# Performance work log

Hardware: AMD Instinct MI355X
Metric: run time of the kernel (lower is better)

Reference implementation:

```python
import jax, jax.numpy as jnp
import numpy as np

B, T, C = 8, 2048, 1024
HEAD = 64

def setup_inputs() -> dict:
    key = jax.random.key(0)
    k1, k2 = jax.random.split(key)
    x = jax.random.normal(k1, (B, T, C), dtype=jnp.float32)
    W_qkv = jax.random.normal(k2, (C, 3 * HEAD), dtype=jnp.float32) * (C ** -0.5)
    return {"x": x, "W_qkv": W_qkv}

def reference(x, W_qkv):
    # qkv projection (bias-free Linear): [B,T,3*HEAD]
    qkv = x @ W_qkv
    q, k, v = jnp.split(qkv, 3, axis=-1)  # each [B,T,HEAD]
    # scaled dot-product scores [B,T,T]
    dots = jnp.einsum('btd,bsd->bts', q, k) * (HEAD ** -0.5)
    # causal mask (tril == keep)
    Tq = x.shape[1]
    causal = jnp.tril(jnp.ones((Tq, Tq), dtype=bool))
    dots = jnp.where(causal, dots, -jnp.inf)
    attn = jax.nn.softmax(dots, axis=-1)
    # dropout p=0.0 (eval) -> identity
    out = jnp.einsum('bts,bsd->btd', attn, v)  # [B,T,HEAD]
    return out
```

## Files before the change

kernel.cpp:

```cpp
#include <hip/hip_runtime.h>
#include <stdint.h>

#define NB 8
#define NT 2048
#define NC 1024
#define HD 64

typedef __attribute__((ext_vector_type(8)))  short s16x8;
typedef __attribute__((ext_vector_type(4)))  float f32x4;
typedef __attribute__((ext_vector_type(16))) float f32x16;

__device__ inline ushort f2b(float f) {
    union { float f; uint32_t u; } c; c.f = f;
    uint32_t u = c.u;
    uint32_t r = (u + 0x7fffu + ((u >> 16) & 1u)) >> 16;
    return (ushort)r;
}

__device__ inline uint32_t cvt_pk_bf16(float lo, float hi) {
    uint32_t r;
    asm("v_cvt_pk_bf16_f32 %0, %1, %2" : "=v"(r) : "v"(lo), "v"(hi));
    return r;
}

__device__ inline void gload_lds16(const void* gsrc, void* lds) {
    __builtin_amdgcn_global_load_lds(
        (const __attribute__((address_space(1))) void*)gsrc,
        (__attribute__((address_space(3))) void*)lds, 16, 0, 0);
}

__global__ __launch_bounds__(256) void wprep(const float* __restrict__ W,
                                             ushort* __restrict__ wt) {
    int tid = blockIdx.x * 256 + threadIdx.x;
    int n = tid >> 10;
    int k = tid & 1023;
    float v = W[k * 192 + n];
    if (n < 64) v *= 0.125f * 1.4426950408889634f;
    wt[n * 1024 + k] = f2b(v);
}

__global__ __launch_bounds__(256, 2) void qkv_gemm(const float* __restrict__ x,
                                                   const ushort* __restrict__ wt,
                                                   ushort* __restrict__ qs,
                                                   ushort* __restrict__ kk,
                                                   ushort* __restrict__ vt) {
    __shared__ __align__(16) char Al[2][16384];
    __shared__ __align__(16) char Wl[2][12288];

    const int tid = threadIdx.x;
    const int wv  = tid >> 6;
    const int ls  = tid & 63;
    const int r16 = ls & 15;
    const int hi4 = ls >> 4;
    const int bid = blockIdx.x;
    const int rowtile = bid & 255;
    const int cg  = bid >> 8;
    const int row0 = rowtile * 64;

    const float* xsrc[4];
#pragma unroll
    for (int j = 0; j < 4; ++j) {
        int r = wv * 16 + j * 4 + (ls >> 4);
        int slot = (ls & 15) ^ (r & 7);
        xsrc[j] = x + (size_t)(row0 + r) * NC + slot * 4;
    }
    const ushort* wsrc[3];
#pragma unroll
    for (int j = 0; j < 3; ++j) {
        int n = wv * 24 + j * 8 + (ls >> 3);
        int slot = (ls & 7) ^ (n & 7);
        wsrc[j] = wt + (size_t)(cg * 96 + n) * 1024 + slot * 8;
    }

    const int key = r16 & 7;
    const int arow = wv * 16 + r16;
    int aoff[2];
#pragma unroll
    for (int kq = 0; kq < 2; ++kq)
        aoff[kq] = arow * 256 + (((kq * 8 + hi4 * 2) ^ key) << 4);
    int bnrow[6];
#pragma unroll
    for (int nf = 0; nf < 6; ++nf)
        bnrow[nf] = (nf * 16 + r16) * 128;
    int bkey[2];
#pragma unroll
    for (int kq = 0; kq < 2; ++kq)
        bkey[kq] = (((kq * 4 + hi4) ^ key) << 4);

    f32x4 acc[6];
#pragma unroll
    for (int j = 0; j < 6; ++j)
#pragma unroll
        for (int e = 0; e < 4; ++e) acc[j][e] = 0.f;

    auto STAGE = [&](int t) {
        int bb = t & 1;
#pragma unroll
        for (int j = 0; j < 4; ++j)
            gload_lds16(xsrc[j] + t * 64, &Al[bb][wv * 4096 + j * 1024]);
#pragma unroll
        for (int j = 0; j < 3; ++j)
            gload_lds16(wsrc[j] + t * 64, &Wl[bb][wv * 3072 + j * 1024]);
    };

    auto COMPUTE = [&](int bb) {
#pragma unroll
        for (int kq = 0; kq < 2; ++kq) {
            float4 a0 = *(const float4*)(&Al[bb][0] + aoff[kq]);
            float4 a1 = *(const float4*)(&Al[bb][0] + (aoff[kq] ^ 16));
            union { uint32_t w[4]; s16x8 v; } pk;
            pk.w[0] = cvt_pk_bf16(a0.x, a0.y);
            pk.w[1] = cvt_pk_bf16(a0.z, a0.w);
            pk.w[2] = cvt_pk_bf16(a1.x, a1.y);
            pk.w[3] = cvt_pk_bf16(a1.z, a1.w);
            s16x8 af = pk.v;
            s16x8 bf[6];
#pragma unroll
            for (int nf = 0; nf < 6; ++nf)
                bf[nf] = *(const s16x8*)(&Wl[bb][0] + bnrow[nf] + bkey[kq]);
#pragma unroll
            for (int nf = 0; nf < 6; ++nf)
                acc[nf] = __builtin_amdgcn_mfma_f32_16x16x32_bf16(
                    af, bf[nf], acc[nf], 0, 0, 0);
        }
    };

    STAGE(0);
    asm volatile("s_waitcnt vmcnt(0)" ::: "memory");
    __builtin_amdgcn_s_barrier();

    for (int t = 0; t < 16; ++t) {
        if (t < 15) STAGE(t + 1);
        COMPUTE(t & 1);
        asm volatile("s_waitcnt vmcnt(0)" ::: "memory");
        __builtin_amdgcn_s_barrier();
    }

    const int b = row0 >> 11;
    const int rbase = row0 + wv * 16 + hi4 * 4;
#pragma unroll
    for (int nf = 0; nf < 6; ++nf) {
        int colg = cg * 96 + nf * 16 + r16;
        f32x4 v = acc[nf];
        if (colg < 64) {
#pragma unroll
            for (int j = 0; j < 4; ++j)
                qs[(size_t)(rbase + j) * HD + colg] = f2b(v[j]);
        } else if (colg < 128) {
#pragma unroll
            for (int j = 0; j < 4; ++j)
                kk[(size_t)(rbase + j) * HD + (colg - 64)] = f2b(v[j]);
        } else {
            int d = colg - 128;
            union { ushort4 s; ushort u[4]; } pk;
#pragma unroll
            for (int j = 0; j < 4; ++j) pk.u[j] = f2b(v[j]);
            *(ushort4*)(&vt[((size_t)(b * 64 + d)) * NT + (rbase & (NT - 1))]) = pk.s;
        }
    }
}

__global__ __launch_bounds__(256) void attn(const ushort* __restrict__ qs,
                                            const ushort* __restrict__ kk,
                                            const ushort* __restrict__ vt,
                                            float* __restrict__ out) {
    __shared__ float ob[4][64][33];
    __shared__ float ml[4][2][32];

    const int bid  = blockIdx.x;
    const int b    = bid & 7;
    const int tile = 63 - (bid >> 3);
    const int tid  = threadIdx.x;
    const int wv   = tid >> 6;
    const int l    = tid & 63;
    const int qcol = l & 31;
    const int hi   = l >> 5;
    const int r0   = tile * 32;

    const ushort* qb = qs + ((size_t)(b * NT + r0)) * HD;
    const ushort* kb = kk + (size_t)b * NT * HD;
    const ushort* vb = vt + (size_t)b * HD * NT;

    s16x8 qf[4];
#pragma unroll
    for (int c = 0; c < 4; ++c)
        qf[c] = *(const s16x8*)(qb + (size_t)qcol * HD + c * 16 + hi * 8);

    f32x16 o0, o1;
#pragma unroll
    for (int i = 0; i < 16; ++i) { o0[i] = 0.f; o1[i] = 0.f; }
    float m = -3.0e30f, lsum = 0.f;

    if (wv <= tile) {
        s16x8 kf[4], vf[4];
        {
            const ushort* kr = kb + (size_t)(wv * 32 + qcol) * HD;
#pragma unroll
            for (int c = 0; c < 4; ++c)
                kf[c] = *(const s16x8*)(kr + c * 16 + hi * 8);
#pragma unroll
            for (int dt = 0; dt < 2; ++dt)
#pragma unroll
                for (int kc = 0; kc < 2; ++kc)
                    vf[dt * 2 + kc] = *(const s16x8*)(vb + (size_t)(dt * 32 + qcol) * NT
                                                      + wv * 32 + kc * 16 + hi * 8);
        }

        for (int kt = wv; kt <= tile; kt += 4) {
            f32x16 s;
#pragma unroll
            for (int i = 0; i < 16; ++i) s[i] = 0.f;
#pragma unroll
            for (int c = 0; c < 4; ++c)
                s = __builtin_amdgcn_mfma_f32_32x32x16_bf16(kf[c], qf[c], s, 0, 0, 0);

            s16x8 kfn[4], vfn[4];
            const bool more = (kt + 4 <= tile);
            if (more) {
                const ushort* kr = kb + (size_t)((kt + 4) * 32 + qcol) * HD;
#pragma unroll
                for (int c = 0; c < 4; ++c)
                    kfn[c] = *(const s16x8*)(kr + c * 16 + hi * 8);
#pragma unroll
                for (int dt = 0; dt < 2; ++dt)
#pragma unroll
                    for (int kc = 0; kc < 2; ++kc)
                        vfn[dt * 2 + kc] = *(const s16x8*)(vb + (size_t)(dt * 32 + qcol) * NT
                                                           + (kt + 4) * 32 + kc * 16 + hi * 8);
            }

            const bool diag = (kt == tile);
            float p[16];
#pragma unroll
            for (int r = 0; r < 16; ++r) {
                int klocal = (r & 3) + 8 * (r >> 2) + 4 * hi;
                float sv = s[r];
                if (diag && klocal > qcol) sv = -3.0e30f;
                p[r] = sv;
            }
            float pmax = p[0];
#pragma unroll
            for (int r = 1; r < 16; ++r) pmax = fmaxf(pmax, p[r]);
            pmax = fmaxf(pmax, __shfl_xor(pmax, 32));
            float mnew = fmaxf(m, pmax);
            float corr = exp2f(m - mnew);
            m = mnew;
            float rs = 0.f;
#pragma unroll
            for (int r = 0; r < 16; ++r) { p[r] = exp2f(p[r] - mnew); rs += p[r]; }
            rs += __shfl_xor(rs, 32);
            lsum = lsum * corr + rs;
#pragma unroll
            for (int i = 0; i < 16; ++i) { o0[i] *= corr; o1[i] *= corr; }

#pragma unroll
            for (int kc = 0; kc < 2; ++kc) {
                int pb = kc * 8;
                uint32_t a0 = cvt_pk_bf16(p[pb + 0], p[pb + 1]);
                uint32_t a1 = cvt_pk_bf16(p[pb + 2], p[pb + 3]);
                uint32_t b0 = cvt_pk_bf16(p[pb + 4], p[pb + 5]);
                uint32_t b1 = cvt_pk_bf16(p[pb + 6], p[pb + 7]);
                uint32_t a0x = __shfl_xor(a0, 32);
                uint32_t a1x = __shfl_xor(a1, 32);
                uint32_t b0x = __shfl_xor(b0, 32);
                uint32_t b1x = __shfl_xor(b1, 32);
                union { uint32_t w[4]; s16x8 v; } frag;
                frag.w[0] = hi ? b0x : a0;
                frag.w[1] = hi ? b1x : a1;
                frag.w[2] = hi ? b0  : a0x;
                frag.w[3] = hi ? b1  : a1x;
                o0 = __builtin_amdgcn_mfma_f32_32x32x16_bf16(vf[0 * 2 + kc], frag.v, o0, 0, 0, 0);
                o1 = __builtin_amdgcn_mfma_f32_32x32x16_bf16(vf[1 * 2 + kc], frag.v, o1, 0, 0, 0);
            }

            if (more) {
#pragma unroll
                for (int c = 0; c < 4; ++c) kf[c] = kfn[c];
#pragma unroll
                for (int c = 0; c < 4; ++c) vf[c] = vfn[c];
            }
        }
    }

#pragma unroll
    for (int r = 0; r < 16; ++r) {
        int d = (r & 3) + 8 * (r >> 2) + 4 * hi;
        ob[wv][d][qcol]      = o0[r];
        ob[wv][d + 32][qcol] = o1[r];
    }
    if (hi == 0) {
        ml[wv][0][qcol] = m;
        ml[wv][1][qcol] = lsum;
    }
    __syncthreads();

    const int q  = tid >> 3;
    const int j0 = (tid & 7) * 8;
    float mw[4];
#pragma unroll
    for (int w = 0; w < 4; ++w) mw[w] = ml[w][0][q];
    float M = fmaxf(fmaxf(mw[0], mw[1]), fmaxf(mw[2], mw[3]));
    float sw[4]; float L = 0.f;
#pragma unroll
    for (int w = 0; w < 4; ++w) {
        sw[w] = exp2f(mw[w] - M);
        L += sw[w] * ml[w][1][q];
    }
    float invL = 1.0f / L;
    float vals[8];
#pragma unroll
    for (int j = 0; j < 8; ++j) {
        int d = j0 + j;
        float acc = 0.f;
#pragma unroll
        for (int w = 0; w < 4; ++w) acc += sw[w] * ob[w][d][q];
        vals[j] = acc * invL;
    }
    float* orow = out + ((size_t)(b * NT + r0 + q)) * HD + j0;
    *(float4*)(orow)     = make_float4(vals[0], vals[1], vals[2], vals[3]);
    *(float4*)(orow + 4) = make_float4(vals[4], vals[5], vals[6], vals[7]);
}

extern "C" void kernel_launch(void* const* d_in, const int* in_sizes, int n_in,
                              void* d_out, int out_size, void* d_ws, size_t ws_size,
                              hipStream_t stream) {
    const float* x = (const float*)d_in[0];
    const float* W = (const float*)d_in[1];
    float* out = (float*)d_out;

    ushort* qs = (ushort*)d_ws;
    ushort* kk = qs + (size_t)NB * NT * HD;
    ushort* vt = kk + (size_t)NB * NT * HD;
    ushort* wt = vt + (size_t)NB * NT * HD;

    wprep<<<768, 256, 0, stream>>>(W, wt);
    qkv_gemm<<<512, 256, 0, stream>>>(x, wt, qs, kk, vt);
    attn<<<512, 256, 0, stream>>>(qs, kk, vt, out);
}
```

Before: 54.20 us.

## Stage x through registers as bf16 and deepen QKV GEMM prefetch

The QKV projection kernel now loads x tiles into registers and converts them to bf16 once before writing them to LDS. Previously fp32 went to LDS and every compute step converted it again, so the A buffer in LDS is halved. The W tiles move to a four-deep LDS ring, and loads are issued two K-steps ahead with a partial vmcnt wait and a single barrier per step. The aim is to hide global-load latency better and cut LDS traffic and conversion work, at the cost of more live registers, which may pressure the two-blocks-per-CU occupancy target.

```diff
diff --git a/kernel.cpp b/kernel.cpp
--- a/kernel.cpp
+++ b/kernel.cpp
@@ -44,8 +44,8 @@
                                                    ushort* __restrict__ qs,
                                                    ushort* __restrict__ kk,
                                                    ushort* __restrict__ vt) {
-    __shared__ __align__(16) char Al[2][16384];
-    __shared__ __align__(16) char Wl[2][12288];
+    __shared__ __align__(16) char Al[2][8192];
+    __shared__ __align__(16) char Wl[4][12288];
 
     const int tid = threadIdx.x;
     const int wv  = tid >> 6;
@@ -57,13 +57,13 @@
     const int cg  = bid >> 8;
     const int row0 = rowtile * 64;
 
-    const float* xsrc[4];
-#pragma unroll
-    for (int j = 0; j < 4; ++j) {
-        int r = wv * 16 + j * 4 + (ls >> 4);
-        int slot = (ls & 15) ^ (r & 7);
-        xsrc[j] = x + (size_t)(row0 + r) * NC + slot * 4;
-    }
+    const int arl = ls >> 2;
+    const int asl = ls & 3;
+    const float* pA = x + (size_t)(row0 + wv * 16 + arl) * NC + asl * 8;
+    const int akey = arl & 7;
+    const int awb0 = (wv * 16 + arl) * 128 + ((asl ^ akey) << 4);
+    const int awb1 = (wv * 16 + arl) * 128 + (((asl + 4) ^ akey) << 4);
+
     const ushort* wsrc[3];
 #pragma unroll
     for (int j = 0; j < 3; ++j) {
@@ -77,7 +77,7 @@
     int aoff[2];
 #pragma unroll
     for (int kq = 0; kq < 2; ++kq)
-        aoff[kq] = arow * 256 + (((kq * 8 + hi4 * 2) ^ key) << 4);
+        aoff[kq] = arow * 128 + (((kq * 4 + hi4) ^ key) << 4);
     int bnrow[6];
 #pragma unroll
     for (int nf = 0; nf < 6; ++nf)
@@ -93,48 +93,73 @@
 #pragma unroll
         for (int e = 0; e < 4; ++e) acc[j][e] = 0.f;
 
-    auto STAGE = [&](int t) {
-        int bb = t & 1;
-#pragma unroll
-        for (int j = 0; j < 4; ++j)
-            gload_lds16(xsrc[j] + t * 64, &Al[bb][wv * 4096 + j * 1024]);
-#pragma unroll
-        for (int j = 0; j < 3; ++j)
-            gload_lds16(wsrc[j] + t * 64, &Wl[bb][wv * 3072 + j * 1024]);
-    };
-
-    auto COMPUTE = [&](int bb) {
-#pragma unroll
-        for (int kq = 0; kq < 2; ++kq) {
-            float4 a0 = *(const float4*)(&Al[bb][0] + aoff[kq]);
-            float4 a1 = *(const float4*)(&Al[bb][0] + (aoff[kq] ^ 16));
-            union { uint32_t w[4]; s16x8 v; } pk;
-            pk.w[0] = cvt_pk_bf16(a0.x, a0.y);
-            pk.w[1] = cvt_pk_bf16(a0.z, a0.w);
-            pk.w[2] = cvt_pk_bf16(a1.x, a1.y);
-            pk.w[3] = cvt_pk_bf16(a1.z, a1.w);
-            s16x8 af = pk.v;
-            s16x8 bf[6];
-#pragma unroll
-            for (int nf = 0; nf < 6; ++nf)
-                bf[nf] = *(const s16x8*)(&Wl[bb][0] + bnrow[nf] + bkey[kq]);
-#pragma unroll
-            for (int nf = 0; nf < 6; ++nf)
-                acc[nf] = __builtin_amdgcn_mfma_f32_16x16x32_bf16(
-                    af, bf[nf], acc[nf], 0, 0, 0);
+    float4 rA[2][4];
+
+#define STAGE_LOAD(T, P)                                                     \
+    do {                                                                     \
+        rA[P][0] = *(const float4*)(pA + (T) * 64);                          \
+        rA[P][1] = *(const float4*)(pA + (T) * 64 + 4);                      \
+        rA[P][2] = *(const float4*)(pA + (T) * 64 + 32);                     \
+        rA[P][3] = *(const float4*)(pA + (T) * 64 + 36);                     \
+        gload_lds16(wsrc[0] + (T) * 64, &Wl[(T) & 3][wv * 3072 + 0 * 1024]); \
+        gload_lds16(wsrc[1] + (T) * 64, &Wl[(T) & 3][wv * 3072 + 1 * 1024]); \
+        gload_lds16(wsrc[2] + (T) * 64, &Wl[(T) & 3][wv * 3072 + 2 * 1024]); \
+    } while (0)
+
+#define A_WRITE(BB, P)                                                       \
+    do {                                                                     \
+        union { uint32_t w[4]; s16x8 v; } p0, p1;                            \
+        p0.w[0] = cvt_pk_bf16(rA[P][0].x, rA[P][0].y);                       \
+        p0.w[1] = cvt_pk_bf16(rA[P][0].z, rA[P][0].w);                       \
+        p0.w[2] = cvt_pk_bf16(rA[P][1].x, rA[P][1].y);                       \
+        p0.w[3] = cvt_pk_bf16(rA[P][1].z, rA[P][1].w);                       \
+        p1.w[0] = cvt_pk_bf16(rA[P][2].x, rA[P][2].y);                       \
+        p1.w[1] = cvt_pk_bf16(rA[P][2].z, rA[P][2].w);                       \
+        p1.w[2] = cvt_pk_bf16(rA[P][3].x, rA[P][3].y);                       \
+        p1.w[3] = cvt_pk_bf16(rA[P][3].z, rA[P][3].w);                       \
+        *(s16x8*)(&Al[BB][awb0]) = p0.v;                                     \
+        *(s16x8*)(&Al[BB][awb1]) = p1.v;                                     \
+    } while (0)
+
+#define COMPUTE(AB, WB)                                                      \
+    do {                                                                     \
+        _Pragma("unroll")                                                    \
+        for (int kq = 0; kq < 2; ++kq) {                                     \
+            s16x8 af = *(const s16x8*)(&Al[AB][0] + aoff[kq]);               \
+            s16x8 bf[6];                                                     \
+            _Pragma("unroll")                                                \
+            for (int nf = 0; nf < 6; ++nf)                                   \
+                bf[nf] = *(const s16x8*)(&Wl[WB][0] + bnrow[nf] + bkey[kq]); \
+            _Pragma("unroll")                                                \
+            for (int nf = 0; nf < 6; ++nf)                                   \
+                acc[nf] = __builtin_amdgcn_mfma_f32_16x16x32_bf16(           \
+                    af, bf[nf], acc[nf], 0, 0, 0);                           \
+        }                                                                    \
+    } while (0)
+
+    STAGE_LOAD(0, 0);
+    STAGE_LOAD(1, 1);
+    asm volatile("s_waitcnt vmcnt(7)" ::: "memory");
+    A_WRITE(0, 0);
+    asm volatile("s_waitcnt lgkmcnt(0)" ::: "memory");
+    __builtin_amdgcn_s_barrier();
+
+#pragma unroll
+    for (int t = 0; t < 16; ++t) {
+        if (t + 2 <= 15) {
+            STAGE_LOAD(t + 2, t & 1);
+            asm volatile("s_waitcnt vmcnt(7)" ::: "memory");
+        } else {
+            asm volatile("s_waitcnt vmcnt(0)" ::: "memory");
         }
-    };
-
-    STAGE(0);
-    asm volatile("s_waitcnt vmcnt(0)" ::: "memory");
-    __builtin_amdgcn_s_barrier();
-
-    for (int t = 0; t < 16; ++t) {
-        if (t < 15) STAGE(t + 1);
-        COMPUTE(t & 1);
-        asm volatile("s_waitcnt vmcnt(0)" ::: "memory");
+        if (t + 1 <= 15) A_WRITE((t + 1) & 1, (t + 1) & 1);
+        asm volatile("s_waitcnt lgkmcnt(0)" ::: "memory");
         __builtin_amdgcn_s_barrier();
-    }
+        COMPUTE(t & 1, t & 3);
+    }
+#undef STAGE_LOAD
+#undef A_WRITE
+#undef COMPUTE
 
     const int b = row0 >> 11;
     const int rbase = row0 + wv * 16 + hi4 * 4;
```

Result: no change. 54.03 us (-0.3%).
